# Optimization experiments

Measured on AMD Instinct MI355X. Metric: run time of the kernel, lower is better.

Reference implementation:

```python
import jax, jax.numpy as jnp
import numpy as np

N = 16384
HID = 256
MI = 128
POS_PER_NODE = 4
TEMP = 0.5


def setup_inputs() -> dict:
    key = jax.random.key(0)
    k1, k2, k3, k4 = jax.random.split(key, 4)
    h_v1 = jax.random.normal(k1, (N, HID), dtype=jnp.float32)
    h_v2 = jax.random.normal(k2, (N, HID), dtype=jnp.float32)
    W = jax.random.normal(k3, (HID, MI), dtype=jnp.float32) * (1.0 / np.sqrt(HID))
    b = jnp.zeros((MI,), dtype=jnp.float32)
    # 4 positives per row -> every row has a nonzero positive count
    pos_row = jnp.repeat(jnp.arange(N, dtype=jnp.int32), POS_PER_NODE)
    pos_col = jax.random.randint(k4, (N * POS_PER_NODE,), 0, N, dtype=jnp.int32)
    return {"h_v1": h_v1, "h_v2": h_v2, "W": W, "b": b,
            "pos_row": pos_row, "pos_col": pos_col}


def _l2norm(x):
    return x / jnp.linalg.norm(x, axis=-1, keepdims=True)


def _cal_loss_mi(e1, e2, pos_row, pos_col):
    # sim_mat[i,j] = <e1_i, e2_j> / T   (N x N, the big intermediate)
    sim = jnp.einsum('ik,jk->ij', e1, e2) / TEMP
    sim = sim - jax.lax.stop_gradient(jnp.max(sim, axis=1, keepdims=True))
    sim = jnp.exp(sim)
    sim_pos = sim[pos_row, pos_col]                      # [E] gather
    row_sum = jnp.sum(sim, axis=1)                       # [N]
    pos_sum = jax.ops.segment_sum(sim_pos, pos_row, num_segments=N)
    denom = (row_sum - pos_sum)[pos_row]                 # [E]
    log_lv = jnp.log(sim_pos / denom)                    # [E]
    pos_cnt = jax.ops.segment_sum(jnp.ones_like(sim_pos), pos_row, num_segments=N)
    per_row = jax.ops.segment_sum(log_lv, pos_row, num_segments=N) / pos_cnt
    return -jnp.mean(per_row)


def reference(h_v1, h_v2, W, b, pos_row, pos_col):
    p1 = _l2norm(jax.nn.relu(h_v1 @ W + b))
    p2 = _l2norm(jax.nn.relu(h_v2 @ W + b))
    loss = 0.5 * (_cal_loss_mi(p1, p2, pos_row, pos_col)
                  + _cal_loss_mi(p2, p1, pos_row, pos_col))
    return loss
```

## Files before the change

kernel.cpp:

```cpp
#include <hip/hip_runtime.h>

typedef unsigned short ushort_t;
typedef unsigned int uint32;
typedef __attribute__((ext_vector_type(8))) short short8;
typedef __attribute__((ext_vector_type(4))) float f32x4;
typedef __attribute__((ext_vector_type(2))) float f32x2;

#define HID 256
#define MI 128
#define ALPHA 2.8853900817779268f
#define LN2F 0.69314718055994531f

__device__ __forceinline__ float bflo(uint32 u) { return __uint_as_float(u << 16); }
__device__ __forceinline__ float bfhi(uint32 u) { return __uint_as_float(u & 0xffff0000u); }
__device__ __forceinline__ ushort_t f2bf(float f) {
  uint32 u = __float_as_uint(f);
  u += 0x7fffu + ((u >> 16) & 1u);
  return (ushort_t)(u >> 16);
}

__global__ __launch_bounds__(256) void prep_kernel(
    const float* __restrict__ W, ushort_t* __restrict__ Wtb,
    float* __restrict__ fbase, int nz, float* __restrict__ out)
{
  int idx = blockIdx.x * 256 + threadIdx.x;
  if (idx < HID * MI) {
    int k = idx >> 7, nn = idx & 127;
    Wtb[nn * HID + k] = f2bf(W[k * MI + nn]);
  }
  if (idx < nz) fbase[idx] = 0.f;
  if (idx == 0) out[0] = 0.f;
}

__global__ __launch_bounds__(256) void proj_kernel(
    const float* __restrict__ h1, const float* __restrict__ h2,
    const ushort_t* __restrict__ Wtb, const float* __restrict__ b,
    ushort_t* __restrict__ p1b, ushort_t* __restrict__ p2b, int n)
{
  int t = threadIdx.x;
  int lane = t & 63, w = t >> 6;
  int lr = lane & 15, lg = lane >> 4;
  long R0 = (long)blockIdx.x * 64;
  const float* src = (R0 < n) ? (h1 + R0 * HID) : (h2 + (R0 - n) * HID);
  ushort_t* dst = (R0 < n) ? (p1b + R0 * MI) : (p2b + (R0 - n) * MI);
  float scale = (R0 < n) ? ALPHA : 1.0f;

  float bb[8];
  #pragma unroll
  for (int ch = 0; ch < 8; ++ch) bb[ch] = b[ch * 16 + lr];

  int row = w * 16 + lr;
  const float* hrow = src + (size_t)row * HID;
  float4 v0[8], v1[8];
  #pragma unroll
  for (int kt = 0; kt < 8; ++kt) {
    v0[kt] = *(const float4*)(hrow + kt * 32 + lg * 8);
    v1[kt] = *(const float4*)(hrow + kt * 32 + lg * 8 + 4);
  }
  short8 afr[8];
  #pragma unroll
  for (int kt = 0; kt < 8; ++kt) {
    short8 a;
    a[0] = (short)f2bf(v0[kt].x); a[1] = (short)f2bf(v0[kt].y);
    a[2] = (short)f2bf(v0[kt].z); a[3] = (short)f2bf(v0[kt].w);
    a[4] = (short)f2bf(v1[kt].x); a[5] = (short)f2bf(v1[kt].y);
    a[6] = (short)f2bf(v1[kt].z); a[7] = (short)f2bf(v1[kt].w);
    afr[kt] = a;
  }

  f32x4 acc[8];
  #pragma unroll
  for (int ch = 0; ch < 8; ++ch) acc[ch] = (f32x4){0.f, 0.f, 0.f, 0.f};
  #pragma unroll
  for (int ch = 0; ch < 8; ++ch) {
    #pragma unroll
    for (int kt = 0; kt < 8; ++kt) {
      short8 bf = *(const short8*)(Wtb + (size_t)(ch * 16 + lr) * HID + kt * 32 + lg * 8);
      acc[ch] = __builtin_amdgcn_mfma_f32_16x16x32_bf16(afr[kt], bf, acc[ch], 0, 0, 0);
    }
  }

  #pragma unroll
  for (int r = 0; r < 4; ++r) {
    float v[8];
    float ss = 0.f;
    #pragma unroll
    for (int ch = 0; ch < 8; ++ch) {
      v[ch] = fmaxf(acc[ch][r] + bb[ch], 0.f);
      ss += v[ch] * v[ch];
    }
    ss += __shfl_xor(ss, 1, 64);
    ss += __shfl_xor(ss, 2, 64);
    ss += __shfl_xor(ss, 4, 64);
    ss += __shfl_xor(ss, 8, 64);
    float rn = rsqrtf(ss) * scale;
    int orow = w * 16 + lg * 4 + r;
    #pragma unroll
    for (int ch = 0; ch < 8; ++ch)
      dst[(size_t)orow * MI + ch * 16 + lr] = f2bf(v[ch] * rn);
  }
}

__global__ __launch_bounds__(256, 2) void sim_kernel(
    const ushort_t* __restrict__ p1b, const ushort_t* __restrict__ p2b,
    float* __restrict__ rowsum, float* __restrict__ colsum,
    const int* __restrict__ pos_row, const int* __restrict__ pos_col,
    float* __restrict__ psum1, float* __restrict__ psum2,
    float* __restrict__ srow1, float* __restrict__ srow2,
    float* __restrict__ cntb, int E)
{
  __shared__ __align__(16) unsigned char ldsB[32768];
  __shared__ float colacc[1024];
  int t = threadIdx.x;
  int lane = t & 63, w = t >> 6;
  int lr = lane & 15, lg = lane >> 4;
  int rowbase = blockIdx.y * 256 + w * 64;
  int jbase = blockIdx.x * 1024;

  uint4 st0, st1, st2, st3;
  int gs = t & 15, r0 = t >> 4;
  int sw = (gs ^ (r0 & 15)) << 4;

  auto load_stage = [&](int jt) {
    int j0 = jbase + jt * 64;
    const ushort_t* base = p2b + (size_t)(j0 + r0) * MI + (gs << 3);
    st0 = *(const uint4*)(base);
    st1 = *(const uint4*)(base + 16 * MI);
    st2 = *(const uint4*)(base + 32 * MI);
    st3 = *(const uint4*)(base + 48 * MI);
  };
  auto write_stage = [&](int buf) {
    unsigned char* base = ldsB + buf * 16384 + r0 * 256 + sw;
    *(uint4*)(base)            = st0;
    *(uint4*)(base + 16 * 256) = st1;
    *(uint4*)(base + 32 * 256) = st2;
    *(uint4*)(base + 48 * 256) = st3;
  };

  load_stage(0);

  short8 afr[4][4];
  #pragma unroll
  for (int rt = 0; rt < 4; ++rt)
    #pragma unroll
    for (int kt = 0; kt < 4; ++kt)
      afr[rt][kt] = *(const short8*)(p1b + (size_t)(rowbase + rt * 16 + lr) * MI + kt * 32 + lg * 8);

  colacc[t] = 0.f;
  colacc[256 + t] = 0.f;
  colacc[512 + t] = 0.f;
  colacc[768 + t] = 0.f;

  f32x2 rs2[4][2];
  #pragma unroll
  for (int rt = 0; rt < 4; ++rt) {
    rs2[rt][0] = (f32x2){0.f, 0.f};
    rs2[rt][1] = (f32x2){0.f, 0.f};
  }

  write_stage(0);
  __syncthreads();

  for (int jt = 0; jt < 16; ++jt) {
    int cur = jt & 1;
    if (jt + 1 < 16) load_stage(jt + 1);
    const unsigned char* B = ldsB + cur * 16384;

    #pragma unroll
    for (int ch = 0; ch < 4; ++ch) {
      f32x4 acc[4];
      #pragma unroll
      for (int rt = 0; rt < 4; ++rt) acc[rt] = (f32x4){0.f, 0.f, 0.f, 0.f};
      #pragma unroll
      for (int kt = 0; kt < 4; ++kt) {
        int ncol = ch * 16 + lr;
        int g = kt * 4 + lg;
        short8 bf = *(const short8*)(B + ncol * 256 + ((g ^ (ncol & 15)) << 4));
        #pragma unroll
        for (int rt = 0; rt < 4; ++rt)
          acc[rt] = __builtin_amdgcn_mfma_f32_16x16x32_bf16(afr[rt][kt], bf, acc[rt], 0, 0, 0);
      }
      f32x2 cs2 = (f32x2){0.f, 0.f};
      #pragma unroll
      for (int rt = 0; rt < 4; ++rt) {
        f32x2 e01, e23;
        e01[0] = __builtin_amdgcn_exp2f(acc[rt][0]);
        e01[1] = __builtin_amdgcn_exp2f(acc[rt][1]);
        e23[0] = __builtin_amdgcn_exp2f(acc[rt][2]);
        e23[1] = __builtin_amdgcn_exp2f(acc[rt][3]);
        rs2[rt][0] += e01;
        rs2[rt][1] += e23;
        cs2 += e01;
        cs2 += e23;
      }
      float csum = cs2[0] + cs2[1];
      csum += __shfl_xor(csum, 16, 64);
      csum += __shfl_xor(csum, 32, 64);
      if (lg == 0) atomicAdd(&colacc[jt * 64 + ch * 16 + lr], csum);
    }
    if (jt + 1 < 16) write_stage(1 - cur);
    __syncthreads();
  }

  #pragma unroll
  for (int rt = 0; rt < 4; ++rt)
    #pragma unroll
    for (int j = 0; j < 2; ++j)
      #pragma unroll
      for (int s = 0; s < 2; ++s) {
        float v = rs2[rt][j][s];
        v += __shfl_xor(v, 1, 64);
        v += __shfl_xor(v, 2, 64);
        v += __shfl_xor(v, 4, 64);
        v += __shfl_xor(v, 8, 64);
        if (lr == 0) atomicAdd(&rowsum[rowbase + rt * 16 + lg * 4 + j * 2 + s], v);
      }

  atomicAdd(&colsum[jbase + t], colacc[t]);
  atomicAdd(&colsum[jbase + 256 + t], colacc[256 + t]);
  atomicAdd(&colsum[jbase + 512 + t], colacc[512 + t]);
  atomicAdd(&colsum[jbase + 768 + t], colacc[768 + t]);

  {
    int eb = blockIdx.y * gridDim.x + blockIdx.x;
    int e = eb * 64 + (t >> 2), q = t & 3;
    if (e < E) {
      int r = pos_row[e], c = pos_col[e];
      const uint4* a1 = (const uint4*)(p1b + (size_t)r * MI) + q * 4;
      const uint4* b1 = (const uint4*)(p2b + (size_t)c * MI) + q * 4;
      const uint4* a2 = (const uint4*)(p1b + (size_t)c * MI) + q * 4;
      const uint4* b2 = (const uint4*)(p2b + (size_t)r * MI) + q * 4;
      float d1 = 0.f, d2 = 0.f;
      #pragma unroll
      for (int it = 0; it < 4; ++it) {
        uint4 x = a1[it], y = b1[it];
        d1 += bflo(x.x) * bflo(y.x) + bfhi(x.x) * bfhi(y.x);
        d1 += bflo(x.y) * bflo(y.y) + bfhi(x.y) * bfhi(y.y);
        d1 += bflo(x.z) * bflo(y.z) + bfhi(x.z) * bfhi(y.z);
        d1 += bflo(x.w) * bflo(y.w) + bfhi(x.w) * bfhi(y.w);
        uint4 u = a2[it], v = b2[it];
        d2 += bflo(u.x) * bflo(v.x) + bfhi(u.x) * bfhi(v.x);
        d2 += bflo(u.y) * bflo(v.y) + bfhi(u.y) * bfhi(v.y);
        d2 += bflo(u.z) * bflo(v.z) + bfhi(u.z) * bfhi(v.z);
        d2 += bflo(u.w) * bflo(v.w) + bfhi(u.w) * bfhi(v.w);
      }
      d1 += __shfl_xor(d1, 1, 64);
      d1 += __shfl_xor(d1, 2, 64);
      d2 += __shfl_xor(d2, 1, 64);
      d2 += __shfl_xor(d2, 2, 64);
      if (q == 0) {
        float e1 = __builtin_amdgcn_exp2f(d1);
        float e2 = __builtin_amdgcn_exp2f(d2);
        atomicAdd(&psum1[r], e1);
        atomicAdd(&srow1[r], d1 * LN2F);
        atomicAdd(&psum2[r], e2);
        atomicAdd(&srow2[r], d2 * LN2F);
        atomicAdd(&cntb[r], 1.0f);
      }
    }
  }
}

__global__ __launch_bounds__(256) void finalize_kernel(
    const float* __restrict__ rowsum, const float* __restrict__ colsum,
    const float* __restrict__ psum1, const float* __restrict__ psum2,
    const float* __restrict__ srow1, const float* __restrict__ srow2,
    const float* __restrict__ cntb, float* __restrict__ out, int n)
{
  __shared__ float sred[4];
  int r = blockIdx.x * 256 + threadIdx.x;
  float local = 0.f;
  if (r < n) {
    float inv = 1.0f / cntb[r];
    float d1 = rowsum[r] - psum1[r];
    float d2 = colsum[r] - psum2[r];
    local = srow1[r] * inv - __builtin_amdgcn_logf(d1) * LN2F
          + srow2[r] * inv - __builtin_amdgcn_logf(d2) * LN2F;
  }
  #pragma unroll
  for (int m = 1; m <= 32; m <<= 1) local += __shfl_xor(local, m, 64);
  int lane = threadIdx.x & 63, wv = threadIdx.x >> 6;
  if (lane == 0) sred[wv] = local;
  __syncthreads();
  if (threadIdx.x == 0) {
    float tot = sred[0] + sred[1] + sred[2] + sred[3];
    atomicAdd(out, -tot / (2.0f * n));
  }
}

extern "C" void kernel_launch(void* const* d_in, const int* in_sizes, int n_in,
                              void* d_out, int out_size, void* d_ws, size_t ws_size,
                              hipStream_t stream)
{
  const float* h1 = (const float*)d_in[0];
  const float* h2 = (const float*)d_in[1];
  const float* W  = (const float*)d_in[2];
  const float* b  = (const float*)d_in[3];
  const int* pos_row = (const int*)d_in[4];
  const int* pos_col = (const int*)d_in[5];
  int n = in_sizes[0] / HID;
  int E = in_sizes[4];
  float* out = (float*)d_out;

  char* ws = (char*)d_ws;
  ushort_t* p1b = (ushort_t*)ws;
  ushort_t* p2b = p1b + (size_t)n * MI;
  float* fbase  = (float*)(ws + (size_t)2 * n * MI * sizeof(ushort_t));
  float* rowsum = fbase;
  float* colsum = rowsum + n;
  float* psum1  = colsum + n;
  float* psum2  = psum1 + n;
  float* srow1  = psum2 + n;
  float* srow2  = srow1 + n;
  float* cntb   = srow2 + n;
  ushort_t* Wtb = (ushort_t*)(cntb + n);

  int nz = 7 * n;
  prep_kernel<<<(nz + 255) / 256, 256, 0, stream>>>(W, Wtb, fbase, nz, out);
  proj_kernel<<<2 * n / 64, 256, 0, stream>>>(h1, h2, Wtb, b, p1b, p2b, n);
  dim3 g2(n / 1024, n / 256);
  sim_kernel<<<g2, 256, 0, stream>>>(p1b, p2b, rowsum, colsum,
                                     pos_row, pos_col, psum1, psum2,
                                     srow1, srow2, cntb, E);
  finalize_kernel<<<(n + 255) / 256, 256, 0, stream>>>(rowsum, colsum, psum1, psum2,
                                                       srow1, srow2, cntb, out, n);
}
```

Before: 195.0 us.

## Fuse weight prep and zero-init into projection kernel via LDS-staged W

```diff
diff --git a/kernel.cpp b/kernel.cpp
--- a/kernel.cpp
+++ b/kernel.cpp
@@ -19,24 +19,13 @@
   return (ushort_t)(u >> 16);
 }
 
-__global__ __launch_bounds__(256) void prep_kernel(
-    const float* __restrict__ W, ushort_t* __restrict__ Wtb,
-    float* __restrict__ fbase, int nz, float* __restrict__ out)
-{
-  int idx = blockIdx.x * 256 + threadIdx.x;
-  if (idx < HID * MI) {
-    int k = idx >> 7, nn = idx & 127;
-    Wtb[nn * HID + k] = f2bf(W[k * MI + nn]);
-  }
-  if (idx < nz) fbase[idx] = 0.f;
-  if (idx == 0) out[0] = 0.f;
-}
-
 __global__ __launch_bounds__(256) void proj_kernel(
     const float* __restrict__ h1, const float* __restrict__ h2,
-    const ushort_t* __restrict__ Wtb, const float* __restrict__ b,
-    ushort_t* __restrict__ p1b, ushort_t* __restrict__ p2b, int n)
+    const float* __restrict__ W, const float* __restrict__ b,
+    ushort_t* __restrict__ p1b, ushort_t* __restrict__ p2b,
+    float* __restrict__ fbase, int nz, float* __restrict__ out, int n)
 {
+  __shared__ __align__(16) unsigned char wt[65536];
   int t = threadIdx.x;
   int lane = t & 63, w = t >> 6;
   int lr = lane & 15, lg = lane >> 4;
@@ -45,6 +34,26 @@
   ushort_t* dst = (R0 < n) ? (p1b + R0 * MI) : (p2b + (R0 - n) * MI);
   float scale = (R0 < n) ? ALPHA : 1.0f;
 
+  {
+    int base = blockIdx.x * 224;
+    if (t < 224 && base + t < nz) fbase[base + t] = 0.f;
+    if (blockIdx.x == 0 && t == 0) out[0] = 0.f;
+  }
+
+  #pragma unroll
+  for (int i = 0; i < 32; ++i) {
+    int idx4 = i * 1024 + t * 4;
+    float4 v = *(const float4*)(W + idx4);
+    int k = idx4 >> 7, nc0 = idx4 & 127;
+    int g = k >> 3, klo = (k & 7) * 2;
+    #pragma unroll
+    for (int j = 0; j < 4; ++j) {
+      int nc = nc0 + j;
+      float f = (j == 0) ? v.x : (j == 1) ? v.y : (j == 2) ? v.z : v.w;
+      *(ushort_t*)(wt + nc * 512 + ((g ^ (nc & 31)) << 4) + klo) = f2bf(f);
+    }
+  }
+
   float bb[8];
   #pragma unroll
   for (int ch = 0; ch < 8; ++ch) bb[ch] = b[ch * 16 + lr];
@@ -68,14 +77,18 @@
     afr[kt] = a;
   }
 
+  __syncthreads();
+
   f32x4 acc[8];
   #pragma unroll
   for (int ch = 0; ch < 8; ++ch) acc[ch] = (f32x4){0.f, 0.f, 0.f, 0.f};
   #pragma unroll
   for (int ch = 0; ch < 8; ++ch) {
+    int ncol = ch * 16 + lr;
     #pragma unroll
     for (int kt = 0; kt < 8; ++kt) {
-      short8 bf = *(const short8*)(Wtb + (size_t)(ch * 16 + lr) * HID + kt * 32 + lg * 8);
+      int g = kt * 4 + lg;
+      short8 bf = *(const short8*)(wt + ncol * 512 + ((g ^ (ncol & 31)) << 4));
       acc[ch] = __builtin_amdgcn_mfma_f32_16x16x32_bf16(afr[kt], bf, acc[ch], 0, 0, 0);
     }
   }
@@ -313,11 +326,10 @@
   float* srow1  = psum2 + n;
   float* srow2  = srow1 + n;
   float* cntb   = srow2 + n;
-  ushort_t* Wtb = (ushort_t*)(cntb + n);
 
   int nz = 7 * n;
-  prep_kernel<<<(nz + 255) / 256, 256, 0, stream>>>(W, Wtb, fbase, nz, out);
-  proj_kernel<<<2 * n / 64, 256, 0, stream>>>(h1, h2, Wtb, b, p1b, p2b, n);
+  proj_kernel<<<2 * n / 64, 256, 0, stream>>>(h1, h2, W, b, p1b, p2b,
+                                              fbase, nz, out, n);
   dim3 g2(n / 1024, n / 256);
   sim_kernel<<<g2, 256, 0, stream>>>(p1b, p2b, rowsum, colsum,
                                      pos_row, pos_col, psum1, psum2,
```

Result: no change. 192.0 us (-1.6%).
